# Kernel tuning notes

Hardware: AMD Instinct MI355X
Metric: run time of the kernel (lower is better)

The kernel has to match this reference:

```python
import jax, jax.numpy as jnp
import numpy as np

V, E, B, NODES_PER_GRAPH = 100000, 128, 4096, 64
N = B * NODES_PER_GRAPH  # 262144 nodes per side
EPS = 1e-6


def setup_inputs() -> dict:
    key = jax.random.key(0)
    k1, k2, k3, k4, k5, k6 = jax.random.split(key, 6)
    left_x = jax.random.randint(k1, (N, 1), 0, V, dtype=jnp.int64 if jax.config.jax_enable_x64 else jnp.int32)
    right_x = jax.random.randint(k2, (N, 1), 0, V, dtype=left_x.dtype)
    # sorted segment ids with every graph non-empty (64 nodes per graph)
    batch_ids = jnp.repeat(jnp.arange(B, dtype=left_x.dtype), NODES_PER_GRAPH)
    label = jax.random.randint(k3, (B,), 0, 2).astype(jnp.float32)
    emb_table = jax.random.normal(k4, (V, E), dtype=jnp.float32)
    W = jax.random.normal(k5, (E, E), dtype=jnp.float32) / np.sqrt(E)
    b = jax.random.normal(k6, (E,), dtype=jnp.float32) * 0.01
    return {
        "left_x": left_x,
        "left_graph_index": jnp.arange(B, dtype=left_x.dtype),
        "right_x": right_x,
        "right_graph_index": jnp.arange(B, dtype=left_x.dtype),
        "left_x_batch": batch_ids,
        "right_x_batch": batch_ids,
        "label": label,
        "emb_table": emb_table,
        "W": W,
        "b": b,
    }


def _side_emb(x, x_batch, emb_table, W, b, num_segments):
    node_emb = emb_table[x[:, 0]]                       # [N, E] gather
    pooled = jax.ops.segment_max(node_emb, x_batch,      # [B, E] scatter-max
                                 num_segments=num_segments,
                                 indices_are_sorted=True)
    return pooled @ W.T + b                              # trans_linear


def reference(left_x, left_graph_index, right_x, right_graph_index,
              left_x_batch, right_x_batch, label, emb_table, W, b):
    num_segments = label.shape[0]
    left_final = _side_emb(left_x, left_x_batch, emb_table, W, b, num_segments)
    right_final = _side_emb(right_x, right_x_batch, emb_table, W, b, num_segments)
    # torch CosineSimilarity(eps=1e-6): clamp each norm at eps
    dot = jnp.sum(left_final * right_final, axis=-1)
    nl = jnp.maximum(jnp.linalg.norm(left_final, axis=-1), EPS)
    nr = jnp.maximum(jnp.linalg.norm(right_final, axis=-1), EPS)
    cos = dot / (nl * nr)                                # [B]
    # ContrastiveLoss(margin=1.0), size_average=True
    losses = 0.5 * ((1.0 - label) * cos ** 2
                    + label * jnp.maximum(1.0 - cos, 0.0) ** 2)
    sim_loss = losses.mean()
    return sim_loss, cos
```

## Files before the change

kernel.cpp:

```cpp
#include <hip/hip_runtime.h>
#include <math.h>

#define B_GRAPHS 4096
#define NPG 64
#define E_DIM 128
#define INV_B (1.0f / 4096.0f)

__global__ __launch_bounds__(256) void fused_graph_sim_k(
    const int* __restrict__ lx, const int* __restrict__ rx,
    const float* __restrict__ emb, const float* __restrict__ W,
    const float* __restrict__ bias, const float* __restrict__ label,
    float* __restrict__ out)
{
    const int g = blockIdx.x;
    const int t = threadIdx.x;

    __shared__ int   idxL[NPG], idxR[NPG];
    __shared__ float4 redL[256], redR[256];
    __shared__ float4 P4[2][32];
    __shared__ float  F[2][E_DIM];

    if (t < NPG)            idxL[t]        = lx[g * NPG + t];
    else if (t < 2 * NPG)   idxR[t - NPG]  = rx[g * NPG + (t - NPG)];
    __syncthreads();

    const int n0 = t >> 5;
    const int q  = t & 31;
    float4 aL = make_float4(-INFINITY, -INFINITY, -INFINITY, -INFINITY);
    float4 aR = aL;
    #pragma unroll
    for (int i = 0; i < 8; ++i) {
        const int n = (i << 3) + n0;
        const float4 vL =
            reinterpret_cast<const float4*>(emb + (size_t)idxL[n] * E_DIM)[q];
        const float4 vR =
            reinterpret_cast<const float4*>(emb + (size_t)idxR[n] * E_DIM)[q];
        aL.x = fmaxf(aL.x, vL.x); aL.y = fmaxf(aL.y, vL.y);
        aL.z = fmaxf(aL.z, vL.z); aL.w = fmaxf(aL.w, vL.w);
        aR.x = fmaxf(aR.x, vR.x); aR.y = fmaxf(aR.y, vR.y);
        aR.z = fmaxf(aR.z, vR.z); aR.w = fmaxf(aR.w, vR.w);
    }
    redL[t] = aL;
    redR[t] = aR;
    __syncthreads();

    if (t < 64) {
        const int side = t >> 5;
        const int qq   = t & 31;
        const float4* __restrict__ src = side ? redR : redL;
        float4 m = src[qq];
        #pragma unroll
        for (int j = 1; j < 8; ++j) {
            const float4 v = src[j * 32 + qq];
            m.x = fmaxf(m.x, v.x); m.y = fmaxf(m.y, v.y);
            m.z = fmaxf(m.z, v.z); m.w = fmaxf(m.w, v.w);
        }
        P4[side][qq] = m;
    }
    __syncthreads();

    {
        const int side = t & 1;
        const int e    = t >> 1;
        float acc = bias[e];
        const float4* __restrict__ wr =
            reinterpret_cast<const float4*>(W + (size_t)e * E_DIM);
        const float4* __restrict__ pv = P4[side];
        #pragma unroll 8
        for (int fi = 0; fi < 32; ++fi) {
            const float4 wv = wr[fi];
            const float4 p  = pv[fi];
            acc = fmaf(p.x, wv.x, acc);
            acc = fmaf(p.y, wv.y, acc);
            acc = fmaf(p.z, wv.z, acc);
            acc = fmaf(p.w, wv.w, acc);
        }
        F[side][e] = acc;
    }
    __syncthreads();

    if (t < 64) {
        const float l0 = F[0][t], l1 = F[0][t + 64];
        const float r0 = F[1][t], r1 = F[1][t + 64];
        float dot = l0 * r0 + l1 * r1;
        float nl  = l0 * l0 + l1 * l1;
        float nr  = r0 * r0 + r1 * r1;
        #pragma unroll
        for (int off = 32; off; off >>= 1) {
            dot += __shfl_down(dot, off);
            nl  += __shfl_down(nl,  off);
            nr  += __shfl_down(nr,  off);
        }
        if (t == 0) {
            const float nlv = fmaxf(sqrtf(nl), 1e-6f);
            const float nrv = fmaxf(sqrtf(nr), 1e-6f);
            const float c   = dot / (nlv * nrv);
            out[1 + g] = c;
            const float lab = label[g];
            const float mm  = fmaxf(1.0f - c, 0.0f);
            const float loss = 0.5f * ((1.0f - lab) * c * c + lab * mm * mm);
            atomicAdd(out, loss * INV_B);
        }
    }
}

extern "C" void kernel_launch(void* const* d_in, const int* in_sizes, int n_in,
                              void* d_out, int out_size, void* d_ws, size_t ws_size,
                              hipStream_t stream)
{
    const int*   lx    = (const int*)d_in[0];
    const int*   rx    = (const int*)d_in[2];
    const float* label = (const float*)d_in[6];
    const float* emb   = (const float*)d_in[7];
    const float* W     = (const float*)d_in[8];
    const float* bias  = (const float*)d_in[9];

    float* out = (float*)d_out;

    hipMemsetAsync(out, 0, sizeof(float), stream);

    fused_graph_sim_k<<<B_GRAPHS, 256, 0, stream>>>(
        lx, rx, emb, W, bias, label, out);
}
```

Before: 160.6 us.

## Issue all gather loads up front and reduce via wave shuffles

Hoists all 16 embedding-row loads per thread ahead of a tree max, so more memory requests are in flight at once. The cross-row max is partly done with a cross-half-wave shuffle instead of shared memory, using a smaller split reduction buffer. The final dot and norm reductions now run across all four waves with shuffles and a small shared array, which drops the F staging buffer. It also adds a waves-per-EU hint to launch_bounds, at the risk of higher register pressure from 16 live float4 values.

```diff
diff --git a/kernel.cpp b/kernel.cpp
--- a/kernel.cpp
+++ b/kernel.cpp
@@ -6,65 +6,98 @@
 #define E_DIM 128
 #define INV_B (1.0f / 4096.0f)
 
-__global__ __launch_bounds__(256) void fused_graph_sim_k(
+static __device__ __forceinline__ float4 fmax4(float4 a, float4 b) {
+    return make_float4(fmaxf(a.x, b.x), fmaxf(a.y, b.y),
+                       fmaxf(a.z, b.z), fmaxf(a.w, b.w));
+}
+
+__global__ __launch_bounds__(256, 6) void fused_graph_sim_k(
     const int* __restrict__ lx, const int* __restrict__ rx,
     const float* __restrict__ emb, const float* __restrict__ W,
     const float* __restrict__ bias, const float* __restrict__ label,
     float* __restrict__ out)
 {
-    const int g = blockIdx.x;
-    const int t = threadIdx.x;
+    const int g    = blockIdx.x;
+    const int t    = threadIdx.x;
+    const int w    = t >> 6;
+    const int lane = t & 63;
 
     __shared__ int   idxL[NPG], idxR[NPG];
-    __shared__ float4 redL[256], redR[256];
+    __shared__ float red[2][4][E_DIM];
     __shared__ float4 P4[2][32];
-    __shared__ float  F[2][E_DIM];
+    __shared__ float wred[3][4];
 
-    if (t < NPG)            idxL[t]        = lx[g * NPG + t];
-    else if (t < 2 * NPG)   idxR[t - NPG]  = rx[g * NPG + (t - NPG)];
+    if (t < NPG)          idxL[t]       = lx[g * NPG + t];
+    else if (t < 2 * NPG) idxR[t - NPG] = rx[g * NPG + (t - NPG)];
     __syncthreads();
 
     const int n0 = t >> 5;
     const int q  = t & 31;
-    float4 aL = make_float4(-INFINITY, -INFINITY, -INFINITY, -INFINITY);
-    float4 aR = aL;
-    #pragma unroll
-    for (int i = 0; i < 8; ++i) {
-        const int n = (i << 3) + n0;
-        const float4 vL =
-            reinterpret_cast<const float4*>(emb + (size_t)idxL[n] * E_DIM)[q];
-        const float4 vR =
-            reinterpret_cast<const float4*>(emb + (size_t)idxR[n] * E_DIM)[q];
-        aL.x = fmaxf(aL.x, vL.x); aL.y = fmaxf(aL.y, vL.y);
-        aL.z = fmaxf(aL.z, vL.z); aL.w = fmaxf(aL.w, vL.w);
-        aR.x = fmaxf(aR.x, vR.x); aR.y = fmaxf(aR.y, vR.y);
-        aR.z = fmaxf(aR.z, vR.z); aR.w = fmaxf(aR.w, vR.w);
+
+    const float4* __restrict__ e4 = reinterpret_cast<const float4*>(emb);
+    float4 l0 = e4[(size_t)idxL[     n0] * 32 + q];
+    float4 l1 = e4[(size_t)idxL[ 8 + n0] * 32 + q];
+    float4 l2 = e4[(size_t)idxL[16 + n0] * 32 + q];
+    float4 l3 = e4[(size_t)idxL[24 + n0] * 32 + q];
+    float4 l4 = e4[(size_t)idxL[32 + n0] * 32 + q];
+    float4 l5 = e4[(size_t)idxL[40 + n0] * 32 + q];
+    float4 l6 = e4[(size_t)idxL[48 + n0] * 32 + q];
+    float4 l7 = e4[(size_t)idxL[56 + n0] * 32 + q];
+    float4 r0 = e4[(size_t)idxR[     n0] * 32 + q];
+    float4 r1 = e4[(size_t)idxR[ 8 + n0] * 32 + q];
+    float4 r2 = e4[(size_t)idxR[16 + n0] * 32 + q];
+    float4 r3 = e4[(size_t)idxR[24 + n0] * 32 + q];
+    float4 r4 = e4[(size_t)idxR[32 + n0] * 32 + q];
+    float4 r5 = e4[(size_t)idxR[40 + n0] * 32 + q];
+    float4 r6 = e4[(size_t)idxR[48 + n0] * 32 + q];
+    float4 r7 = e4[(size_t)idxR[56 + n0] * 32 + q];
+
+    float4 aL = fmax4(fmax4(fmax4(l0, l1), fmax4(l2, l3)),
+                      fmax4(fmax4(l4, l5), fmax4(l6, l7)));
+    float4 aR = fmax4(fmax4(fmax4(r0, r1), fmax4(r2, r3)),
+                      fmax4(fmax4(r4, r5), fmax4(r6, r7)));
+
+    aL.x = fmaxf(aL.x, __shfl_xor(aL.x, 32));
+    aL.y = fmaxf(aL.y, __shfl_xor(aL.y, 32));
+    aL.z = fmaxf(aL.z, __shfl_xor(aL.z, 32));
+    aL.w = fmaxf(aL.w, __shfl_xor(aL.w, 32));
+    aR.x = fmaxf(aR.x, __shfl_xor(aR.x, 32));
+    aR.y = fmaxf(aR.y, __shfl_xor(aR.y, 32));
+    aR.z = fmaxf(aR.z, __shfl_xor(aR.z, 32));
+    aR.w = fmaxf(aR.w, __shfl_xor(aR.w, 32));
+
+    if (lane < 32) {
+        const int o = w * 32 + lane;
+        red[0][0][o] = aL.x; red[0][1][o] = aL.y;
+        red[0][2][o] = aL.z; red[0][3][o] = aL.w;
+        red[1][0][o] = aR.x; red[1][1][o] = aR.y;
+        red[1][2][o] = aR.z; red[1][3][o] = aR.w;
     }
-    redL[t] = aL;
-    redR[t] = aR;
     __syncthreads();
 
     if (t < 64) {
         const int side = t >> 5;
         const int qq   = t & 31;
-        const float4* __restrict__ src = side ? redR : redL;
-        float4 m = src[qq];
-        #pragma unroll
-        for (int j = 1; j < 8; ++j) {
-            const float4 v = src[j * 32 + qq];
-            m.x = fmaxf(m.x, v.x); m.y = fmaxf(m.y, v.y);
-            m.z = fmaxf(m.z, v.z); m.w = fmaxf(m.w, v.w);
-        }
+        float4 m;
+        m.x = fmaxf(fmaxf(red[side][0][qq],      red[side][0][32 + qq]),
+                    fmaxf(red[side][0][64 + qq], red[side][0][96 + qq]));
+        m.y = fmaxf(fmaxf(red[side][1][qq],      red[side][1][32 + qq]),
+                    fmaxf(red[side][1][64 + qq], red[side][1][96 + qq]));
+        m.z = fmaxf(fmaxf(red[side][2][qq],      red[side][2][32 + qq]),
+                    fmaxf(red[side][2][64 + qq], red[side][2][96 + qq]));
+        m.w = fmaxf(fmaxf(red[side][3][qq],      red[side][3][32 + qq]),
+                    fmaxf(red[side][3][64 + qq], red[side][3][96 + qq]));
         P4[side][qq] = m;
     }
     __syncthreads();
 
+    float acc;
     {
         const int side = t & 1;
         const int e    = t >> 1;
-        float acc = bias[e];
+        acc = bias[e];
         const float4* __restrict__ wr =
-            reinterpret_cast<const float4*>(W + (size_t)e * E_DIM);
+            reinterpret_cast<const float4*>(W) + (size_t)e * 32;
         const float4* __restrict__ pv = P4[side];
         #pragma unroll 8
         for (int fi = 0; fi < 32; ++fi) {
@@ -75,32 +108,39 @@
             acc = fmaf(p.z, wv.z, acc);
             acc = fmaf(p.w, wv.w, acc);
         }
-        F[side][e] = acc;
+    }
+
+    {
+        const float other = __shfl_xor(acc, 1);
+        const float l = (t & 1) ? other : acc;
+        const float r = (t & 1) ? acc   : other;
+        float dot = l * r;
+        float nl  = l * l;
+        float nr  = r * r;
+        #pragma unroll
+        for (int off = 1; off < 64; off <<= 1) {
+            dot += __shfl_xor(dot, off);
+            nl  += __shfl_xor(nl,  off);
+            nr  += __shfl_xor(nr,  off);
+        }
+        if (lane == 0) {
+            wred[0][w] = dot; wred[1][w] = nl; wred[2][w] = nr;
+        }
     }
     __syncthreads();
 
-    if (t < 64) {
-        const float l0 = F[0][t], l1 = F[0][t + 64];
-        const float r0 = F[1][t], r1 = F[1][t + 64];
-        float dot = l0 * r0 + l1 * r1;
-        float nl  = l0 * l0 + l1 * l1;
-        float nr  = r0 * r0 + r1 * r1;
-        #pragma unroll
-        for (int off = 32; off; off >>= 1) {
-            dot += __shfl_down(dot, off);
-            nl  += __shfl_down(nl,  off);
-            nr  += __shfl_down(nr,  off);
-        }
-        if (t == 0) {
-            const float nlv = fmaxf(sqrtf(nl), 1e-6f);
-            const float nrv = fmaxf(sqrtf(nr), 1e-6f);
-            const float c   = dot / (nlv * nrv);
-            out[1 + g] = c;
-            const float lab = label[g];
-            const float mm  = fmaxf(1.0f - c, 0.0f);
-            const float loss = 0.5f * ((1.0f - lab) * c * c + lab * mm * mm);
-            atomicAdd(out, loss * INV_B);
-        }
+    if (t == 0) {
+        const float dd = 0.5f * (wred[0][0] + wred[0][1] + wred[0][2] + wred[0][3]);
+        const float ll = 0.5f * (wred[1][0] + wred[1][1] + wred[1][2] + wred[1][3]);
+        const float rr = 0.5f * (wred[2][0] + wred[2][1] + wred[2][2] + wred[2][3]);
+        const float nlv = fmaxf(sqrtf(ll), 1e-6f);
+        const float nrv = fmaxf(sqrtf(rr), 1e-6f);
+        const float c   = dd / (nlv * nrv);
+        out[1 + g] = c;
+        const float lab = label[g];
+        const float mm  = fmaxf(1.0f - c, 0.0f);
+        const float loss = 0.5f * ((1.0f - lab) * c * c + lab * mm * mm);
+        atomicAdd(out, loss * INV_B);
     }
 }
 
```

New measurement: 165.2 us. +2.9%, slower.
